# Kernel tuning notes

Measured on AMD Instinct MI355X. Metric: run time of the kernel, lower is better.

The kernel has to match this reference:

```python
import jax, jax.numpy as jnp
import numpy as np
import math

D = 2048
H = 16
DPH = 128          # d_pre_head (nope head dim, also dc_v)
DR = DPH // 2      # d_rope = 64
DC_V = DPH         # 128
DC_KV = DPH // 8   # 16
DC_Q = D // 4      # 512
QHD = DPH + DR     # 192
MEG = DPH + DC_V   # 256
B = 2
S = 2048
EPS = 1e-7


def setup_inputs() -> dict:
    key = jax.random.key(0)
    ks = jax.random.split(key, 8)
    sd = 0.02
    inputs = jax.random.normal(ks[0], (B, S, D), dtype=jnp.float32)
    pos_ids = jnp.tile(jnp.arange(S, dtype=jnp.int64 if jax.config.jax_enable_x64 else jnp.int32), (B, 1))
    mask = jnp.tril(jnp.ones((S, S), dtype=bool))  # causal: True = attend
    return {
        "inputs": inputs,
        "pos_ids": pos_ids,
        "mask": mask,
        "Wq_down": sd * jax.random.normal(ks[1], (D, DC_Q), jnp.float32),
        "q_norm_w": jnp.ones((DC_Q,), jnp.float32),
        "Wq_up": sd * jax.random.normal(ks[2], (DC_Q, H * QHD), jnp.float32),
        "Wkv_down": sd * jax.random.normal(ks[3], (D, DC_KV + DR), jnp.float32),
        "kv_norm_w": jnp.ones((DC_KV,), jnp.float32),
        "Wkv_up": sd * jax.random.normal(ks[4], (DC_KV, H * MEG), jnp.float32),
        "Wout": sd * jax.random.normal(ks[5], (H * DC_V, D), jnp.float32),
    }


def rms_norm(x, w):
    xf = x.astype(jnp.float32)
    var = jnp.mean(xf * xf, axis=-1, keepdims=True)
    return w * (xf * jax.lax.rsqrt(var + EPS)).astype(x.dtype)


def rope_reshape(x):
    # interleaved -> half-split layout: (..., d//2, 2) -> (..., 2, d//2) -> (..., d)
    *lead, d = x.shape
    return jnp.swapaxes(x.reshape(*lead, d // 2, 2), -1, -2).reshape(*lead, d)


def rope_rotate(x):
    h = x.shape[-1] // 2
    return jnp.concatenate([-x[..., h:], x[..., :h]], axis=-1)


def make_cos_sin(pos_ids):
    # pos_ids: [B, S] -> cos/sin: [B, 1, S, DR]
    inv_freq = 1.0 / (10000.0 ** (jnp.arange(0, DR, 2, dtype=jnp.float32) / DR))
    freqs = pos_ids[..., None].astype(jnp.float32) * inv_freq  # [B,S,DR/2]
    emb = jnp.concatenate([freqs, freqs], axis=-1)             # [B,S,DR]
    return jnp.cos(emb)[:, None], jnp.sin(emb)[:, None]


def reference(inputs, pos_ids, mask, Wq_down, q_norm_w, Wq_up, Wkv_down, kv_norm_w, Wkv_up, Wout):
    b, s, _ = inputs.shape
    # Q low-rank path
    q = rms_norm(inputs @ Wq_down, q_norm_w) @ Wq_up                 # [B,S,H*QHD]
    q = q.reshape(b, s, H, QHD).transpose(0, 2, 1, 3)                # [B,H,S,QHD]
    q_nope, q_rope = q[..., :DPH], q[..., DPH:]
    # KV low-rank path (shared latent + decoupled rope key)
    ckv = inputs @ Wkv_down                                          # [B,S,DC_KV+DR]
    c_kv, k_rope = ckv[..., :DC_KV], ckv[..., DC_KV:]
    c_kv = rms_norm(c_kv, kv_norm_w)
    kv = (c_kv @ Wkv_up).reshape(b, s, H, MEG).transpose(0, 2, 1, 3)  # [B,H,S,MEG]
    k_nope, value = kv[..., :DPH], kv[..., DPH:]
    k_rope = k_rope.reshape(b, s, 1, DR).transpose(0, 2, 1, 3)       # [B,1,S,DR]
    # RoPE on rope sub-dims only
    cos, sin = make_cos_sin(pos_ids)
    q_r = rope_reshape(q_rope)
    k_r = rope_reshape(k_rope)
    q_emb = q_r * cos + rope_rotate(q_r) * sin
    k_emb = k_r * cos + rope_rotate(k_r) * sin
    query = jnp.concatenate([q_nope, q_emb], axis=-1)                # [B,H,S,QHD]
    key = jnp.concatenate([k_nope, jnp.broadcast_to(k_emb, (b, H, s, DR))], axis=-1)
    # SDPA with default scale 1/sqrt(QHD), bool mask (True=keep)
    scores = jnp.einsum('bhqd,bhkd->bhqk', query, key) * (1.0 / math.sqrt(QHD))
    scores = jnp.where(mask, scores, -jnp.inf)
    attn = jax.nn.softmax(scores, axis=-1)
    out = jnp.einsum('bhqk,bhkv->bhqv', attn, value)                 # [B,H,S,DC_V]
    out = out.transpose(0, 2, 1, 3).reshape(b, s, H * DC_V)
    return out @ Wout                                                # [B,S,D]
```

## Files before the change

kernel.cpp:

```cpp
#include <hip/hip_runtime.h>

typedef __bf16 bf16;
typedef __bf16 bf16x8 __attribute__((ext_vector_type(8)));
typedef __bf16 bf16x4 __attribute__((ext_vector_type(4)));
typedef float f32x4 __attribute__((ext_vector_type(4)));

constexpr int D = 2048, H = 16, DPH = 128, DR = 64, DC_KV = 16, DC_Q = 512;
constexpr int QHD = 192, MEG = 256, B = 2, S = 2048;
constexpr int T = B * S;
constexpr int NDNP = 640;
constexpr int NQX = 1280;
constexpr float EPS = 1e-7f;
constexpr float KSC = 0.104124247f;

static __device__ __forceinline__ bf16x8 zero8() {
  bf16x8 v;
#pragma unroll
  for (int j = 0; j < 8; j++) v[j] = (bf16)0.f;
  return v;
}

static __device__ __forceinline__ void gload_lds16(const bf16* g, bf16* l) {
  __builtin_amdgcn_global_load_lds(
      (const __attribute__((address_space(1))) unsigned int*)g,
      (__attribute__((address_space(3))) unsigned int*)l, 16, 0, 0);
}

#define LGWAIT0 do { asm volatile("s_waitcnt lgkmcnt(0)" ::: "memory"); __builtin_amdgcn_sched_barrier(0); } while (0)
#define VMWAIT0 do { asm volatile("s_waitcnt vmcnt(0)" ::: "memory"); __builtin_amdgcn_sched_barrier(0); } while (0)

__global__ void rope_table_kernel(float* __restrict__ cos_t, float* __restrict__ sin_t) {
  int i = blockIdx.x * 64 + threadIdx.x;
  int pos = i >> 5, j = i & 31;
  double invf = pow(10000.0, -(double)(2 * j) / 64.0);
  double a = (double)pos * invf;
  cos_t[i] = (float)cos(a);
  sin_t[i] = (float)sin(a);
}

__global__ void zero_bf16_kernel(bf16* __restrict__ p, int n) {
  int i = (blockIdx.x * 256 + threadIdx.x) * 8;
  if (i < n) *reinterpret_cast<bf16x8*>(p + i) = zero8();
}

__global__ void cast_bf16_kernel(const float* __restrict__ in, bf16* __restrict__ out, int n) {
  int i = (blockIdx.x * blockDim.x + threadIdx.x) * 4;
  if (i < n) {
    float4 v = *reinterpret_cast<const float4*>(in + i);
    bf16x4 o;
    o[0] = (bf16)v.x; o[1] = (bf16)v.y; o[2] = (bf16)v.z; o[3] = (bf16)v.w;
    *reinterpret_cast<bf16x4*>(out + i) = o;
  }
}

__global__ __launch_bounds__(256) void transpose_cast_kernel(
    const float* __restrict__ in, bf16* __restrict__ out, int K, int N, int ldo) {
  __shared__ float tile[32][33];
  int k0 = blockIdx.y * 32, n0 = blockIdx.x * 32;
  int tid = threadIdx.x;
#pragma unroll
  for (int e = tid; e < 1024; e += 256) {
    int i = e >> 5, j = e & 31;
    int k = k0 + i, n = n0 + j;
    tile[i][j] = (k < K && n < N) ? in[(size_t)k * N + n] : 0.f;
  }
  __syncthreads();
#pragma unroll
  for (int e = tid; e < 1024; e += 256) {
    int jj = e >> 5, ii = e & 31;
    int n = n0 + jj, k = k0 + ii;
    if (k < K && n < N) out[(size_t)n * ldo + k] = (bf16)tile[ii][jj];
  }
}

__global__ __launch_bounds__(128) void prep_w2_kernel(
    const float* __restrict__ Wkv_up, const float* __restrict__ Wout,
    bf16* __restrict__ W2T) {
  __shared__ float wv[128][16];
  int h = blockIdx.y, d0 = blockIdx.x * 128;
  int tid = threadIdx.x;
#pragma unroll
  for (int e = tid; e < 2048; e += 128) {
    int v = e >> 4, c = e & 15;
    wv[v][c] = Wkv_up[(size_t)c * (H * MEG) + h * MEG + 128 + v];
  }
  __syncthreads();
  int d = d0 + tid;
  float acc[16] = {};
  for (int v = 0; v < 128; v++) {
    float wo = Wout[(size_t)(h * 128 + v) * D + d];
    float4 a0 = *reinterpret_cast<const float4*>(&wv[v][0]);
    float4 a1 = *reinterpret_cast<const float4*>(&wv[v][4]);
    float4 a2 = *reinterpret_cast<const float4*>(&wv[v][8]);
    float4 a3 = *reinterpret_cast<const float4*>(&wv[v][12]);
    acc[0] += a0.x * wo;  acc[1] += a0.y * wo;  acc[2] += a0.z * wo;  acc[3] += a0.w * wo;
    acc[4] += a1.x * wo;  acc[5] += a1.y * wo;  acc[6] += a1.z * wo;  acc[7] += a1.w * wo;
    acc[8] += a2.x * wo;  acc[9] += a2.y * wo;  acc[10] += a2.z * wo; acc[11] += a2.w * wo;
    acc[12] += a3.x * wo; acc[13] += a3.y * wo; acc[14] += a3.z * wo; acc[15] += a3.w * wo;
  }
  bf16x8 o0, o1;
#pragma unroll
  for (int c = 0; c < 8; c++) { o0[c] = (bf16)acc[c]; o1[c] = (bf16)acc[8 + c]; }
  *reinterpret_cast<bf16x8*>(&W2T[(size_t)d * 256 + h * 16]) = o0;
  *reinterpret_cast<bf16x8*>(&W2T[(size_t)d * 256 + h * 16 + 8]) = o1;
}

__global__ __launch_bounds__(128) void prep_w3_kernel(
    const float* __restrict__ Wq_up, const float* __restrict__ Wkv_up,
    bf16* __restrict__ WqxT) {
  __shared__ float wk[128][16];
  int h = blockIdx.y, k0 = blockIdx.x * 128;
  int tid = threadIdx.x;
#pragma unroll
  for (int e = tid; e < 2048; e += 128) {
    int v = e >> 4, c = e & 15;
    wk[v][c] = Wkv_up[(size_t)c * (H * MEG) + h * MEG + v];
  }
  __syncthreads();
  int k = k0 + tid;
  float acc[16] = {};
  for (int v = 0; v < 128; v++) {
    float wq = Wq_up[(size_t)k * (H * QHD) + h * QHD + v];
    float4 a0 = *reinterpret_cast<const float4*>(&wk[v][0]);
    float4 a1 = *reinterpret_cast<const float4*>(&wk[v][4]);
    float4 a2 = *reinterpret_cast<const float4*>(&wk[v][8]);
    float4 a3 = *reinterpret_cast<const float4*>(&wk[v][12]);
    acc[0] += a0.x * wq;  acc[1] += a0.y * wq;  acc[2] += a0.z * wq;  acc[3] += a0.w * wq;
    acc[4] += a1.x * wq;  acc[5] += a1.y * wq;  acc[6] += a1.z * wq;  acc[7] += a1.w * wq;
    acc[8] += a2.x * wq;  acc[9] += a2.y * wq;  acc[10] += a2.z * wq; acc[11] += a2.w * wq;
    acc[12] += a3.x * wq; acc[13] += a3.y * wq; acc[14] += a3.z * wq; acc[15] += a3.w * wq;
  }
#pragma unroll
  for (int c = 0; c < 16; c++)
    WqxT[(size_t)(h * 16 + c) * DC_Q + k] = (bf16)acc[c];
}

__global__ __launch_bounds__(256) void prep_wrope_kernel(
    const float* __restrict__ Wq_up, bf16* __restrict__ WqxT) {
  __shared__ float tile[64][65];
  int h = blockIdx.y, k0 = blockIdx.x * 64;
  int tid = threadIdx.x;
#pragma unroll
  for (int p = 0; p < 16; p++) {
    int kk = p * 4 + (tid >> 6), j = tid & 63;
    tile[kk][j] = Wq_up[(size_t)(k0 + kk) * (H * QHD) + h * QHD + 128 + j];
  }
  __syncthreads();
#pragma unroll
  for (int p = 0; p < 16; p++) {
    int n = p * 4 + (tid >> 6), k = tid & 63;
    WqxT[(size_t)(256 + h * 64 + n) * DC_Q + k0 + k] = (bf16)tile[k][n];
  }
}

__global__ __launch_bounds__(256) void rmsnorm_q_kernel(
    const float* __restrict__ cq, const float* __restrict__ w, bf16* __restrict__ outp, int ld) {
  int wid = threadIdx.x >> 6, lane = threadIdx.x & 63;
  int t = blockIdx.x * 4 + wid;
  const float* x = cq + (size_t)t * ld;
  float4 v0 = *reinterpret_cast<const float4*>(x + lane * 8);
  float4 v1 = *reinterpret_cast<const float4*>(x + lane * 8 + 4);
  float ss = v0.x * v0.x + v0.y * v0.y + v0.z * v0.z + v0.w * v0.w +
             v1.x * v1.x + v1.y * v1.y + v1.z * v1.z + v1.w * v1.w;
#pragma unroll
  for (int off = 32; off; off >>= 1) ss += __shfl_xor(ss, off);
  float r = rsqrtf(ss / (float)DC_Q + EPS);
  const float* wp = w + lane * 8;
  float vv[8] = {v0.x, v0.y, v0.z, v0.w, v1.x, v1.y, v1.z, v1.w};
  bf16x8 o;
#pragma unroll
  for (int j = 0; j < 8; j++) o[j] = (bf16)(vv[j] * r * wp[j]);
  *reinterpret_cast<bf16x8*>(outp + (size_t)t * DC_Q + lane * 8) = o;
}

__global__ __launch_bounds__(64) void kv_prep_kernel(
    const float* __restrict__ cqkv, const float* __restrict__ kvw,
    const int* __restrict__ pos_ids,
    const float* __restrict__ cos_t, const float* __restrict__ sin_t,
    bf16* __restrict__ KcG, bf16* __restrict__ cTG) {
  int t = blockIdx.x;
  int lane = threadIdx.x;
  int b = t >> 11, s = t & (S - 1);
  const float* x = cqkv + (size_t)t * NDNP + DC_Q;
  float v = (lane < 16) ? x[lane] : 0.f;
  float ss = v * v;
#pragma unroll
  for (int off = 1; off < 16; off <<= 1) ss += __shfl_xor(ss, off);
  float r = rsqrtf(ss / 16.f + EPS);
  bf16* krow = KcG + ((size_t)t << 7);
  if (lane < 16) {
    bf16 cn = (bf16)(v * r * kvw[lane]);
    krow[64 + lane] = cn;
    cTG[(size_t)(b * 16 + lane) * S + s] = cn;
  } else {
    krow[64 + lane] = (bf16)0.f;
  }
  if (lane < 32) {
    int j = lane;
    int pos = pos_ids[t];
    float cf = cos_t[pos * 32 + j], sf = sin_t[pos * 32 + j];
    float x0 = x[16 + 2 * j], x1 = x[16 + 2 * j + 1];
    krow[j]      = (bf16)(x0 * cf - x1 * sf);
    krow[32 + j] = (bf16)(x1 * cf + x0 * sf);
  }
}

__global__ __launch_bounds__(256) void build_q_kernel(
    const bf16* __restrict__ qx, const int* __restrict__ pos_ids,
    const float* __restrict__ cos_t, const float* __restrict__ sin_t,
    bf16* __restrict__ Qp) {
  int t = blockIdx.x;
  int b = t >> 11, s = t & (S - 1);
  int tid = threadIdx.x;
  int pos = pos_ids[t];
  const bf16* qr = qx + (size_t)t * NQX;
#pragma unroll
  for (int rep = 0; rep < 2; rep++) {
    int item = rep * 256 + tid;
    int h = item >> 5, j = item & 31;
    float cf = cos_t[pos * 32 + j], sf = sin_t[pos * 32 + j];
    float x0 = (float)qr[256 + h * 64 + 2 * j], x1 = (float)qr[256 + h * 64 + 2 * j + 1];
    bf16* qrow = Qp + (size_t)((b * 16 + h) * 2048 + s) * 96;
    qrow[j]      = (bf16)((x0 * cf - x1 * sf) * KSC);
    qrow[32 + j] = (bf16)((x1 * cf + x0 * sf) * KSC);
  }
  {
    int h = tid >> 4, c = tid & 15;
    bf16* qrow = Qp + (size_t)((b * 16 + h) * 2048 + s) * 96;
    qrow[64 + c] = (bf16)((float)qr[h * 16 + c] * KSC);
    qrow[80 + c] = (bf16)0.f;
  }
}

template <typename OutT>
__global__ __launch_bounds__(256) void gemm_bt_kernel(
    const bf16* __restrict__ A, const bf16* __restrict__ Bt,
    OutT* __restrict__ C, int M, int N, int K) {
  __shared__ bf16 As[2][64 * 64];
  __shared__ bf16 Bs[2][128 * 64];
  int tid = threadIdx.x;
  int wid = tid >> 6, lane = tid & 63;
  int g = lane >> 4, c = lane & 15;
  int nbx = gridDim.x;
  int lin = blockIdx.y * nbx + blockIdx.x;
  int cpx = (nbx * gridDim.y) >> 3;
  int swz = (lin & 7) * cpx + (lin >> 3);
  int m0 = (swz / nbx) * 64, n0 = (swz % nbx) * 128;
  int lrow8 = tid >> 3, lslot = tid & 7;

  auto stage = [&](int kt, int buf) {
    int k0 = kt << 6;
#pragma unroll
    for (int r = 0; r < 2; r++) {
      int row = r * 32 + lrow8;
      int sslot = lslot ^ (row & 7);
      gload_lds16(A + (size_t)(m0 + row) * K + k0 + sslot * 8, &As[buf][row * 64 + lslot * 8]);
    }
#pragma unroll
    for (int r = 0; r < 4; r++) {
      int row = r * 32 + lrow8;
      int sslot = lslot ^ (row & 7);
      gload_lds16(Bt + (size_t)(n0 + row) * K + k0 + sslot * 8, &Bs[buf][row * 64 + lslot * 8]);
    }
  };

  f32x4 acc[4][2] = {};
  int nk = K >> 6;
  stage(0, 0);
  __builtin_amdgcn_sched_barrier(0);
  for (int kt = 0; kt < nk; kt++) {
    int cur = kt & 1;
    __builtin_amdgcn_s_barrier();
    __builtin_amdgcn_sched_barrier(0);
    if (kt + 1 < nk) {
      stage(kt + 1, cur ^ 1);
      asm volatile("s_waitcnt vmcnt(6)" ::: "memory");
    } else {
      asm volatile("s_waitcnt vmcnt(0)" ::: "memory");
    }
    __builtin_amdgcn_sched_barrier(0);
    __builtin_amdgcn_s_barrier();
    __builtin_amdgcn_sched_barrier(0);
#pragma unroll
    for (int kk = 0; kk < 2; kk++) {
      bf16x8 af[4], bfr[2];
#pragma unroll
      for (int mi = 0; mi < 4; mi++) {
        int row = mi * 16 + c;
        int sl = (kk * 4 + g) ^ (row & 7);
        af[mi] = *reinterpret_cast<const bf16x8*>(&As[cur][row * 64 + sl * 8]);
      }
#pragma unroll
      for (int ni = 0; ni < 2; ni++) {
        int row = wid * 32 + ni * 16 + c;
        int sl = (kk * 4 + g) ^ (row & 7);
        bfr[ni] = *reinterpret_cast<const bf16x8*>(&Bs[cur][row * 64 + sl * 8]);
      }
#pragma unroll
      for (int mi = 0; mi < 4; mi++)
#pragma unroll
        for (int ni = 0; ni < 2; ni++)
          acc[mi][ni] = __builtin_amdgcn_mfma_f32_16x16x32_bf16(af[mi], bfr[ni], acc[mi][ni], 0, 0, 0);
    }
  }
#pragma unroll
  for (int mi = 0; mi < 4; mi++)
#pragma unroll
    for (int ni = 0; ni < 2; ni++)
#pragma unroll
      for (int r = 0; r < 4; r++) {
        int row = m0 + mi * 16 + g * 4 + r;
        int col = n0 + wid * 32 + ni * 16 + c;
        C[(size_t)row * N + col] = (OutT)acc[mi][ni][r];
      }
}

__global__ __launch_bounds__(512, 4) void attn_kernel(
    const bf16* __restrict__ Qp, const bf16* __restrict__ KcG,
    const bf16* __restrict__ cTG, bf16* __restrict__ OC) {
  __shared__ bf16 Kls[128 * 128];
  __shared__ bf16 Cls[2][16 * 128];
  __shared__ bf16 Pls[8][16 * 128];

  int lin = blockIdx.x;
  int v = lin >> 8, u = lin & 255;
  int qt = v ? (u >> 1) : (127 - (u >> 1));
  int hg = u & 1, b = v;
  int q0 = qt * 16;
  int nt = qt / 8 + 1;
  int tid = threadIdx.x;
  int w = tid >> 6, lane = tid & 63;
  int g = lane >> 4, cc = lane & 15;
  int h = hg * 8 + w;
  char* pbase = reinterpret_cast<char*>(&Pls[w][0]);

  bf16x8 kst[4];
  auto load_k = [&](int k0) {
#pragma unroll
    for (int i = 0; i < 4; i++) {
      int id = w * 4 + i;
      int key = id * 4 + (lane >> 4);
      int sg = (lane & 15) ^ ((id >> 1) & 15);
      kst[i] = *reinterpret_cast<const bf16x8*>(
          KcG + (((size_t)(b * S + k0 + key)) << 7) + sg * 8);
    }
  };
  auto write_k = [&]() {
#pragma unroll
    for (int i = 0; i < 4; i++) {
      int id = w * 4 + i;
      *reinterpret_cast<bf16x8*>(&Kls[(id * 64 + lane) * 8]) = kst[i];
    }
  };
  auto stage_c = [&](int k0, int buf) {
    if (w >= 4) {
      int c = (w - 4) * 4 + (lane >> 4);
      int sg = (lane & 15) ^ c;
      gload_lds16(cTG + (size_t)(b * 16 + c) * S + k0 + sg * 8,
                  &Cls[buf][(w - 4) * 512]);
    }
  };

  bf16x8 aq[3];
  const bf16* qp = Qp + (size_t)((b * 16 + h) * 2048 + q0 + cc) * 96;
#pragma unroll
  for (int kk = 0; kk < 3; kk++)
    aq[kk] = *reinterpret_cast<const bf16x8*>(qp + kk * 32 + g * 8);

  stage_c(0, 0);
  __builtin_amdgcn_sched_barrier(0);
  load_k(0);
  VMWAIT0;
  write_k();
  if (nt > 1) {
    stage_c(128, 1);
    __builtin_amdgcn_sched_barrier(0);
    load_k(128);
  }
  LGWAIT0;
  __builtin_amdgcn_s_barrier();
  __builtin_amdgcn_sched_barrier(0);

  bf16x8 ones;
#pragma unroll
  for (int j = 0; j < 8; j++) ones[j] = (bf16)1.f;

  f32x4 oc = {}, ls = {};

#pragma unroll 1
  for (int kt = 0; kt < nt; kt++) {
    int cur = kt & 1;
    int k0 = kt * 128;
    f32x4 sacc[8] = {};
    __builtin_amdgcn_s_setprio(1);
#pragma unroll
    for (int kk = 0; kk < 3; kk++)
#pragma unroll
      for (int ntb = 0; ntb < 8; ntb++) {
        int key = cc * 8 + ntb;
        bf16x8 bk = *reinterpret_cast<const bf16x8*>(
            &Kls[(key * 16 + ((kk * 4 + g) ^ cc)) * 8]);
        sacc[ntb] = __builtin_amdgcn_mfma_f32_16x16x32_bf16(aq[kk], bk, sacc[ntb], 0, 0, 0);
      }
    __builtin_amdgcn_s_setprio(0);

    bool diag = (kt == nt - 1);
#pragma unroll
    for (int r = 0; r < 4; r++) {
      bf16x8 pk;
#pragma unroll
      for (int ntb = 0; ntb < 8; ntb++) {
        float x = sacc[ntb][r];
        if (diag) {
          int qr = q0 + g * 4 + r, kc = k0 + cc * 8 + ntb;
          if (kc > qr) x = -1e30f;
        }
        pk[ntb] = (bf16)__builtin_amdgcn_exp2f(x);
      }
      int q = g * 4 + r;
      *reinterpret_cast<bf16x8*>(pbase + (q * 16 + (cc ^ (q & 7))) * 16) = pk;
    }
    LGWAIT0;
    __builtin_amdgcn_s_setprio(1);
#pragma unroll
    for (int kk2 = 0; kk2 < 4; kk2++) {
      bf16x8 pa = *reinterpret_cast<const bf16x8*>(
          pbase + (cc * 16 + ((kk2 * 4 + g) ^ (cc & 7))) * 16);
      bf16x8 bv = *reinterpret_cast<const bf16x8*>(
          &Cls[cur][(cc * 16 + ((kk2 * 4 + g) ^ cc)) * 8]);
      oc = __builtin_amdgcn_mfma_f32_16x16x32_bf16(pa, bv, oc, 0, 0, 0);
      ls = __builtin_amdgcn_mfma_f32_16x16x32_bf16(pa, ones, ls, 0, 0, 0);
    }
    __builtin_amdgcn_s_setprio(0);

    if (kt + 1 < nt) {
      __builtin_amdgcn_s_barrier();
      __builtin_amdgcn_sched_barrier(0);
      VMWAIT0;
      write_k();
      if (kt + 2 < nt) {
        stage_c((kt + 2) * 128, cur);
        __builtin_amdgcn_sched_barrier(0);
        load_k((kt + 2) * 128);
      }
      LGWAIT0;
      __builtin_amdgcn_s_barrier();
      __builtin_amdgcn_sched_barrier(0);
    }
  }

#pragma unroll
  for (int r = 0; r < 4; r++) {
    size_t t = (size_t)b * S + q0 + g * 4 + r;
    OC[t * 256 + h * 16 + cc] = (bf16)(oc[r] / ls[r]);
  }
}

extern "C" void kernel_launch(void* const* d_in, const int* in_sizes, int n_in,
                              void* d_out, int out_size, void* d_ws, size_t ws_size,
                              hipStream_t stream) {
  const float* inputs    = (const float*)d_in[0];
  const int*   pos_ids   = (const int*)d_in[1];
  const float* Wq_down   = (const float*)d_in[3];
  const float* q_norm_w  = (const float*)d_in[4];
  const float* Wq_up     = (const float*)d_in[5];
  const float* Wkv_down  = (const float*)d_in[6];
  const float* kv_norm_w = (const float*)d_in[7];
  const float* Wkv_up    = (const float*)d_in[8];
  const float* Wout      = (const float*)d_in[9];
  float* out = (float*)d_out;

  char* ws = (char*)d_ws;
  size_t off = 0;
  auto alloc = [&](size_t bytes) -> void* {
    void* p = ws + off;
    off += (bytes + 255) & ~(size_t)255;
    return p;
  };

  bf16*  in_bf = (bf16*)alloc((size_t)T * D * 2);
  bf16*  WdT   = (bf16*)alloc((size_t)NDNP * D * 2);
  bf16*  WqxT  = (bf16*)alloc((size_t)NQX * DC_Q * 2);
  bf16*  W2T   = (bf16*)alloc((size_t)D * 256 * 2);
  float* cqkv  = (float*)alloc((size_t)T * NDNP * 4);
  bf16*  cqn   = (bf16*)alloc((size_t)T * DC_Q * 2);
  bf16*  qx    = (bf16*)alloc((size_t)T * NQX * 2);
  bf16*  KcG   = (bf16*)alloc((size_t)T * 128 * 2);
  bf16*  cTG   = (bf16*)alloc((size_t)B * 16 * S * 2);
  bf16*  Qp    = (bf16*)alloc((size_t)B * H * S * 96 * 2);
  bf16*  OC    = (bf16*)alloc((size_t)T * H * 16 * 2);
  float* cos_t = (float*)alloc((size_t)S * 32 * 4);
  float* sin_t = (float*)alloc((size_t)S * 32 * 4);

  rope_table_kernel<<<S * 32 / 64, 64, 0, stream>>>(cos_t, sin_t);
  cast_bf16_kernel<<<(T * D / 4 + 255) / 256, 256, 0, stream>>>(inputs, in_bf, T * D);
  zero_bf16_kernel<<<(NDNP * D / 8 + 255) / 256, 256, 0, stream>>>(WdT, NDNP * D);
  transpose_cast_kernel<<<dim3((DC_Q + 31) / 32, (D + 31) / 32), 256, 0, stream>>>(Wq_down, WdT, D, DC_Q, D);
  transpose_cast_kernel<<<dim3((80 + 31) / 32, (D + 31) / 32), 256, 0, stream>>>(Wkv_down, WdT + (size_t)DC_Q * D, D, 80, D);
  prep_w3_kernel<<<dim3(4, 16), 128, 0, stream>>>(Wq_up, Wkv_up, WqxT);
  prep_wrope_kernel<<<dim3(8, 16), 256, 0, stream>>>(Wq_up, WqxT);
  prep_w2_kernel<<<dim3(16, 16), 128, 0, stream>>>(Wkv_up, Wout, W2T);

  gemm_bt_kernel<float><<<dim3(NDNP / 128, T / 64), 256, 0, stream>>>(in_bf, WdT, cqkv, T, NDNP, D);
  rmsnorm_q_kernel<<<T / 4, 256, 0, stream>>>(cqkv, q_norm_w, cqn, NDNP);
  kv_prep_kernel<<<T, 64, 0, stream>>>(cqkv, kv_norm_w, pos_ids, cos_t, sin_t, KcG, cTG);
  gemm_bt_kernel<bf16><<<dim3(NQX / 128, T / 64), 256, 0, stream>>>(cqn, WqxT, qx, T, NQX, DC_Q);
  build_q_kernel<<<T, 256, 0, stream>>>(qx, pos_ids, cos_t, sin_t, Qp);
  attn_kernel<<<512, 512, 0, stream>>>(Qp, KcG, cTG, OC);
  gemm_bt_kernel<float><<<dim3(D / 128, T / 64), 256, 0, stream>>>(OC, W2T, out, T, D, 256);
}
```

Measured before the change: 154.8 us.

## Merge prep kernels into one prologue and fuse RoPE Q-build into GEMM epilogue

Eight small weight-prep, cast and rope-table launches become a single prologue kernel that dispatches on block index. The Q rmsnorm and KV prep kernels are merged into one. The Q up-projection GEMM now applies RoPE and scaling in its epilogue and writes straight into the attention layout, so the qx intermediate and the build_q kernel go away. This cuts launch count and an HBM round trip, at the cost of scattered 2-byte epilogue stores and only partial zeroing of WdT.

```diff
diff --git a/kernel.cpp b/kernel.cpp
--- a/kernel.cpp
+++ b/kernel.cpp
@@ -29,135 +29,130 @@
 #define LGWAIT0 do { asm volatile("s_waitcnt lgkmcnt(0)" ::: "memory"); __builtin_amdgcn_sched_barrier(0); } while (0)
 #define VMWAIT0 do { asm volatile("s_waitcnt vmcnt(0)" ::: "memory"); __builtin_amdgcn_sched_barrier(0); } while (0)
 
-__global__ void rope_table_kernel(float* __restrict__ cos_t, float* __restrict__ sin_t) {
-  int i = blockIdx.x * 64 + threadIdx.x;
-  int pos = i >> 5, j = i & 31;
-  double invf = pow(10000.0, -(double)(2 * j) / 64.0);
-  double a = (double)pos * invf;
-  cos_t[i] = (float)cos(a);
-  sin_t[i] = (float)sin(a);
-}
-
-__global__ void zero_bf16_kernel(bf16* __restrict__ p, int n) {
-  int i = (blockIdx.x * 256 + threadIdx.x) * 8;
-  if (i < n) *reinterpret_cast<bf16x8*>(p + i) = zero8();
-}
-
-__global__ void cast_bf16_kernel(const float* __restrict__ in, bf16* __restrict__ out, int n) {
-  int i = (blockIdx.x * blockDim.x + threadIdx.x) * 4;
-  if (i < n) {
-    float4 v = *reinterpret_cast<const float4*>(in + i);
+__global__ __launch_bounds__(256) void prologue_kernel(
+    const float* __restrict__ inputs, const float* __restrict__ Wq_down,
+    const float* __restrict__ Wq_up, const float* __restrict__ Wkv_down,
+    const float* __restrict__ Wkv_up, const float* __restrict__ Wout,
+    bf16* __restrict__ in_bf, bf16* __restrict__ WdT, bf16* __restrict__ WqxT,
+    bf16* __restrict__ W2T, float* __restrict__ cos_t, float* __restrict__ sin_t) {
+  __shared__ float smem[64 * 65];
+  int bid = blockIdx.x;
+  int tid = threadIdx.x;
+
+  if (bid < 8192) {
+    int i = (bid * 256 + tid) * 4;
+    float4 v = *reinterpret_cast<const float4*>(inputs + i);
     bf16x4 o;
     o[0] = (bf16)v.x; o[1] = (bf16)v.y; o[2] = (bf16)v.z; o[3] = (bf16)v.w;
-    *reinterpret_cast<bf16x4*>(out + i) = o;
-  }
-}
-
-__global__ __launch_bounds__(256) void transpose_cast_kernel(
-    const float* __restrict__ in, bf16* __restrict__ out, int K, int N, int ldo) {
-  __shared__ float tile[32][33];
-  int k0 = blockIdx.y * 32, n0 = blockIdx.x * 32;
-  int tid = threadIdx.x;
-#pragma unroll
-  for (int e = tid; e < 1024; e += 256) {
-    int i = e >> 5, j = e & 31;
-    int k = k0 + i, n = n0 + j;
-    tile[i][j] = (k < K && n < N) ? in[(size_t)k * N + n] : 0.f;
-  }
-  __syncthreads();
-#pragma unroll
-  for (int e = tid; e < 1024; e += 256) {
-    int jj = e >> 5, ii = e & 31;
-    int n = n0 + jj, k = k0 + ii;
-    if (k < K && n < N) out[(size_t)n * ldo + k] = (bf16)tile[ii][jj];
-  }
-}
-
-__global__ __launch_bounds__(128) void prep_w2_kernel(
-    const float* __restrict__ Wkv_up, const float* __restrict__ Wout,
-    bf16* __restrict__ W2T) {
-  __shared__ float wv[128][16];
-  int h = blockIdx.y, d0 = blockIdx.x * 128;
-  int tid = threadIdx.x;
-#pragma unroll
-  for (int e = tid; e < 2048; e += 128) {
-    int v = e >> 4, c = e & 15;
-    wv[v][c] = Wkv_up[(size_t)c * (H * MEG) + h * MEG + 128 + v];
-  }
-  __syncthreads();
-  int d = d0 + tid;
-  float acc[16] = {};
-  for (int v = 0; v < 128; v++) {
-    float wo = Wout[(size_t)(h * 128 + v) * D + d];
-    float4 a0 = *reinterpret_cast<const float4*>(&wv[v][0]);
-    float4 a1 = *reinterpret_cast<const float4*>(&wv[v][4]);
-    float4 a2 = *reinterpret_cast<const float4*>(&wv[v][8]);
-    float4 a3 = *reinterpret_cast<const float4*>(&wv[v][12]);
-    acc[0] += a0.x * wo;  acc[1] += a0.y * wo;  acc[2] += a0.z * wo;  acc[3] += a0.w * wo;
-    acc[4] += a1.x * wo;  acc[5] += a1.y * wo;  acc[6] += a1.z * wo;  acc[7] += a1.w * wo;
-    acc[8] += a2.x * wo;  acc[9] += a2.y * wo;  acc[10] += a2.z * wo; acc[11] += a2.w * wo;
-    acc[12] += a3.x * wo; acc[13] += a3.y * wo; acc[14] += a3.z * wo; acc[15] += a3.w * wo;
-  }
-  bf16x8 o0, o1;
-#pragma unroll
-  for (int c = 0; c < 8; c++) { o0[c] = (bf16)acc[c]; o1[c] = (bf16)acc[8 + c]; }
-  *reinterpret_cast<bf16x8*>(&W2T[(size_t)d * 256 + h * 16]) = o0;
-  *reinterpret_cast<bf16x8*>(&W2T[(size_t)d * 256 + h * 16 + 8]) = o1;
-}
-
-__global__ __launch_bounds__(128) void prep_w3_kernel(
-    const float* __restrict__ Wq_up, const float* __restrict__ Wkv_up,
-    bf16* __restrict__ WqxT) {
-  __shared__ float wk[128][16];
-  int h = blockIdx.y, k0 = blockIdx.x * 128;
-  int tid = threadIdx.x;
-#pragma unroll
-  for (int e = tid; e < 2048; e += 128) {
-    int v = e >> 4, c = e & 15;
-    wk[v][c] = Wkv_up[(size_t)c * (H * MEG) + h * MEG + v];
-  }
-  __syncthreads();
-  int k = k0 + tid;
-  float acc[16] = {};
-  for (int v = 0; v < 128; v++) {
-    float wq = Wq_up[(size_t)k * (H * QHD) + h * QHD + v];
-    float4 a0 = *reinterpret_cast<const float4*>(&wk[v][0]);
-    float4 a1 = *reinterpret_cast<const float4*>(&wk[v][4]);
-    float4 a2 = *reinterpret_cast<const float4*>(&wk[v][8]);
-    float4 a3 = *reinterpret_cast<const float4*>(&wk[v][12]);
-    acc[0] += a0.x * wq;  acc[1] += a0.y * wq;  acc[2] += a0.z * wq;  acc[3] += a0.w * wq;
-    acc[4] += a1.x * wq;  acc[5] += a1.y * wq;  acc[6] += a1.z * wq;  acc[7] += a1.w * wq;
-    acc[8] += a2.x * wq;  acc[9] += a2.y * wq;  acc[10] += a2.z * wq; acc[11] += a2.w * wq;
-    acc[12] += a3.x * wq; acc[13] += a3.y * wq; acc[14] += a3.z * wq; acc[15] += a3.w * wq;
-  }
-#pragma unroll
-  for (int c = 0; c < 16; c++)
-    WqxT[(size_t)(h * 16 + c) * DC_Q + k] = (bf16)acc[c];
-}
-
-__global__ __launch_bounds__(256) void prep_wrope_kernel(
-    const float* __restrict__ Wq_up, bf16* __restrict__ WqxT) {
-  __shared__ float tile[64][65];
-  int h = blockIdx.y, k0 = blockIdx.x * 64;
-  int tid = threadIdx.x;
-#pragma unroll
-  for (int p = 0; p < 16; p++) {
-    int kk = p * 4 + (tid >> 6), j = tid & 63;
-    tile[kk][j] = Wq_up[(size_t)(k0 + kk) * (H * QHD) + h * QHD + 128 + j];
-  }
-  __syncthreads();
-#pragma unroll
-  for (int p = 0; p < 16; p++) {
-    int n = p * 4 + (tid >> 6), k = tid & 63;
-    WqxT[(size_t)(256 + h * 64 + n) * DC_Q + k0 + k] = (bf16)tile[k][n];
-  }
-}
-
-__global__ __launch_bounds__(256) void rmsnorm_q_kernel(
-    const float* __restrict__ cq, const float* __restrict__ w, bf16* __restrict__ outp, int ld) {
-  int wid = threadIdx.x >> 6, lane = threadIdx.x & 63;
-  int t = blockIdx.x * 4 + wid;
-  const float* x = cq + (size_t)t * ld;
+    *reinterpret_cast<bf16x4*>(in_bf + i) = o;
+  } else if (bid < 8240) {
+    size_t i = (size_t)592 * D + ((size_t)(bid - 8192) * 256 + tid) * 8;
+    *reinterpret_cast<bf16x8*>(WdT + i) = zero8();
+  } else if (bid < 9456) {
+    const float* src; bf16* dst; int K, N, k0, n0;
+    if (bid < 9264) {
+      int lb = bid - 8240;
+      src = Wq_down; dst = WdT; K = D; N = DC_Q;
+      k0 = (lb >> 4) * 32; n0 = (lb & 15) * 32;
+    } else {
+      int lb = bid - 9264;
+      src = Wkv_down; dst = WdT + (size_t)DC_Q * D; K = D; N = 80;
+      k0 = (lb / 3) * 32; n0 = (lb % 3) * 32;
+    }
+    float (*tile)[33] = (float(*)[33])smem;
+#pragma unroll
+    for (int e = tid; e < 1024; e += 256) {
+      int i = e >> 5, j = e & 31;
+      int k = k0 + i, n = n0 + j;
+      tile[i][j] = (k < K && n < N) ? src[(size_t)k * N + n] : 0.f;
+    }
+    __syncthreads();
+#pragma unroll
+    for (int e = tid; e < 1024; e += 256) {
+      int jj = e >> 5, ii = e & 31;
+      int n = n0 + jj, k = k0 + ii;
+      if (k < K && n < N) dst[(size_t)n * D + k] = (bf16)tile[ii][jj];
+    }
+  } else if (bid < 9520) {
+    int lb = bid - 9456;
+    int h = lb >> 2, k0 = (lb & 3) * 128;
+    float (*wk)[16] = (float(*)[16])smem;
+#pragma unroll
+    for (int e = tid; e < 2048; e += 256) {
+      int v = e >> 4, c = e & 15;
+      wk[v][c] = Wkv_up[(size_t)c * (H * MEG) + h * MEG + v];
+    }
+    __syncthreads();
+    if (tid < 128) {
+      int k = k0 + tid;
+      float acc[16] = {};
+      for (int v = 0; v < 128; v++) {
+        float wq = Wq_up[(size_t)k * (H * QHD) + h * QHD + v];
+#pragma unroll
+        for (int c = 0; c < 16; c++) acc[c] += wk[v][c] * wq;
+      }
+#pragma unroll
+      for (int c = 0; c < 16; c++)
+        WqxT[(size_t)(h * 16 + c) * DC_Q + k] = (bf16)acc[c];
+    }
+  } else if (bid < 9648) {
+    int lb = bid - 9520;
+    int h = lb >> 3, k0 = (lb & 7) * 64;
+    float (*tile)[65] = (float(*)[65])smem;
+#pragma unroll
+    for (int p = 0; p < 16; p++) {
+      int kk = p * 4 + (tid >> 6), j = tid & 63;
+      tile[kk][j] = Wq_up[(size_t)(k0 + kk) * (H * QHD) + h * QHD + 128 + j];
+    }
+    __syncthreads();
+#pragma unroll
+    for (int p = 0; p < 16; p++) {
+      int n = p * 4 + (tid >> 6), k = tid & 63;
+      WqxT[(size_t)(256 + h * 64 + n) * DC_Q + k0 + k] = (bf16)tile[k][n];
+    }
+  } else if (bid < 9904) {
+    int lb = bid - 9648;
+    int h = lb >> 4, d0 = (lb & 15) * 128;
+    float (*wv)[16] = (float(*)[16])smem;
+#pragma unroll
+    for (int e = tid; e < 2048; e += 256) {
+      int v = e >> 4, c = e & 15;
+      wv[v][c] = Wkv_up[(size_t)c * (H * MEG) + h * MEG + 128 + v];
+    }
+    __syncthreads();
+    if (tid < 128) {
+      int d = d0 + tid;
+      float acc[16] = {};
+      for (int v = 0; v < 128; v++) {
+        float wo = Wout[(size_t)(h * 128 + v) * D + d];
+#pragma unroll
+        for (int c = 0; c < 16; c++) acc[c] += wv[v][c] * wo;
+      }
+      bf16x8 o0, o1;
+#pragma unroll
+      for (int c = 0; c < 8; c++) { o0[c] = (bf16)acc[c]; o1[c] = (bf16)acc[8 + c]; }
+      *reinterpret_cast<bf16x8*>(&W2T[(size_t)d * 256 + h * 16]) = o0;
+      *reinterpret_cast<bf16x8*>(&W2T[(size_t)d * 256 + h * 16 + 8]) = o1;
+    }
+  } else {
+    int i = (bid - 9904) * 256 + tid;
+    int pos = i >> 5, j = i & 31;
+    double invf = pow(10000.0, -(double)(2 * j) / 64.0);
+    double a = (double)pos * invf;
+    cos_t[i] = (float)cos(a);
+    sin_t[i] = (float)sin(a);
+  }
+}
+
+__global__ __launch_bounds__(256) void norm_kv_kernel(
+    const float* __restrict__ cqkv, const float* __restrict__ qw,
+    const float* __restrict__ kvw, const int* __restrict__ pos_ids,
+    const float* __restrict__ cos_t, const float* __restrict__ sin_t,
+    bf16* __restrict__ cqn, bf16* __restrict__ KcG, bf16* __restrict__ cTG) {
+  int w = threadIdx.x >> 6, lane = threadIdx.x & 63;
+  int t = blockIdx.x * 4 + w;
+  int b = t >> 11, s = t & (S - 1);
+  const float* x = cqkv + (size_t)t * NDNP;
   float4 v0 = *reinterpret_cast<const float4*>(x + lane * 8);
   float4 v1 = *reinterpret_cast<const float4*>(x + lane * 8 + 4);
   float ss = v0.x * v0.x + v0.y * v0.y + v0.z * v0.z + v0.w * v0.w +
@@ -165,31 +160,21 @@
 #pragma unroll
   for (int off = 32; off; off >>= 1) ss += __shfl_xor(ss, off);
   float r = rsqrtf(ss / (float)DC_Q + EPS);
-  const float* wp = w + lane * 8;
+  const float* wp = qw + lane * 8;
   float vv[8] = {v0.x, v0.y, v0.z, v0.w, v1.x, v1.y, v1.z, v1.w};
   bf16x8 o;
 #pragma unroll
   for (int j = 0; j < 8; j++) o[j] = (bf16)(vv[j] * r * wp[j]);
-  *reinterpret_cast<bf16x8*>(outp + (size_t)t * DC_Q + lane * 8) = o;
-}
-
-__global__ __launch_bounds__(64) void kv_prep_kernel(
-    const float* __restrict__ cqkv, const float* __restrict__ kvw,
-    const int* __restrict__ pos_ids,
-    const float* __restrict__ cos_t, const float* __restrict__ sin_t,
-    bf16* __restrict__ KcG, bf16* __restrict__ cTG) {
-  int t = blockIdx.x;
-  int lane = threadIdx.x;
-  int b = t >> 11, s = t & (S - 1);
-  const float* x = cqkv + (size_t)t * NDNP + DC_Q;
-  float v = (lane < 16) ? x[lane] : 0.f;
-  float ss = v * v;
-#pragma unroll
-  for (int off = 1; off < 16; off <<= 1) ss += __shfl_xor(ss, off);
-  float r = rsqrtf(ss / 16.f + EPS);
+  *reinterpret_cast<bf16x8*>(cqn + (size_t)t * DC_Q + lane * 8) = o;
+  const float* xk = x + DC_Q;
+  float vk = (lane < 16) ? xk[lane] : 0.f;
+  float sk = vk * vk;
+#pragma unroll
+  for (int off = 1; off < 16; off <<= 1) sk += __shfl_xor(sk, off);
+  float rk = rsqrtf(sk / 16.f + EPS);
   bf16* krow = KcG + ((size_t)t << 7);
   if (lane < 16) {
-    bf16 cn = (bf16)(v * r * kvw[lane]);
+    bf16 cn = (bf16)(vk * rk * kvw[lane]);
     krow[64 + lane] = cn;
     cTG[(size_t)(b * 16 + lane) * S + s] = cn;
   } else {
@@ -199,43 +184,20 @@
     int j = lane;
     int pos = pos_ids[t];
     float cf = cos_t[pos * 32 + j], sf = sin_t[pos * 32 + j];
-    float x0 = x[16 + 2 * j], x1 = x[16 + 2 * j + 1];
+    float x0 = xk[16 + 2 * j], x1 = xk[16 + 2 * j + 1];
     krow[j]      = (bf16)(x0 * cf - x1 * sf);
     krow[32 + j] = (bf16)(x1 * cf + x0 * sf);
   }
 }
 
-__global__ __launch_bounds__(256) void build_q_kernel(
-    const bf16* __restrict__ qx, const int* __restrict__ pos_ids,
-    const float* __restrict__ cos_t, const float* __restrict__ sin_t,
-    bf16* __restrict__ Qp) {
-  int t = blockIdx.x;
-  int b = t >> 11, s = t & (S - 1);
-  int tid = threadIdx.x;
-  int pos = pos_ids[t];
-  const bf16* qr = qx + (size_t)t * NQX;
-#pragma unroll
-  for (int rep = 0; rep < 2; rep++) {
-    int item = rep * 256 + tid;
-    int h = item >> 5, j = item & 31;
-    float cf = cos_t[pos * 32 + j], sf = sin_t[pos * 32 + j];
-    float x0 = (float)qr[256 + h * 64 + 2 * j], x1 = (float)qr[256 + h * 64 + 2 * j + 1];
-    bf16* qrow = Qp + (size_t)((b * 16 + h) * 2048 + s) * 96;
-    qrow[j]      = (bf16)((x0 * cf - x1 * sf) * KSC);
-    qrow[32 + j] = (bf16)((x1 * cf + x0 * sf) * KSC);
-  }
-  {
-    int h = tid >> 4, c = tid & 15;
-    bf16* qrow = Qp + (size_t)((b * 16 + h) * 2048 + s) * 96;
-    qrow[64 + c] = (bf16)((float)qr[h * 16 + c] * KSC);
-    qrow[80 + c] = (bf16)0.f;
-  }
-}
-
-template <typename OutT>
+template <typename OutT, int EPI>
 __global__ __launch_bounds__(256) void gemm_bt_kernel(
     const bf16* __restrict__ A, const bf16* __restrict__ Bt,
-    OutT* __restrict__ C, int M, int N, int K) {
+    OutT* __restrict__ C, int M, int N, int K,
+    const int* __restrict__ pos_ids = nullptr,
+    const float* __restrict__ cos_t = nullptr,
+    const float* __restrict__ sin_t = nullptr,
+    bf16* __restrict__ Qp = nullptr) {
   __shared__ bf16 As[2][64 * 64];
   __shared__ bf16 Bs[2][128 * 64];
   int tid = threadIdx.x;
@@ -303,16 +265,51 @@
           acc[mi][ni] = __builtin_amdgcn_mfma_f32_16x16x32_bf16(af[mi], bfr[ni], acc[mi][ni], 0, 0, 0);
     }
   }
-#pragma unroll
-  for (int mi = 0; mi < 4; mi++)
-#pragma unroll
-    for (int ni = 0; ni < 2; ni++)
+
+  if constexpr (EPI == 0) {
+#pragma unroll
+    for (int mi = 0; mi < 4; mi++)
+#pragma unroll
+      for (int ni = 0; ni < 2; ni++)
+#pragma unroll
+        for (int r = 0; r < 4; r++) {
+          int row = m0 + mi * 16 + g * 4 + r;
+          int col = n0 + wid * 32 + ni * 16 + c;
+          C[(size_t)row * N + col] = (OutT)acc[mi][ni][r];
+        }
+  } else {
+    bool ropeTile = (n0 >= 256);
+#pragma unroll
+    for (int mi = 0; mi < 4; mi++)
 #pragma unroll
       for (int r = 0; r < 4; r++) {
         int row = m0 + mi * 16 + g * 4 + r;
-        int col = n0 + wid * 32 + ni * 16 + c;
-        C[(size_t)row * N + col] = (OutT)acc[mi][ni][r];
-      }
+        int b = row >> 11, s = row & (S - 1);
+#pragma unroll
+        for (int ni = 0; ni < 2; ni++) {
+          int col = n0 + wid * 32 + ni * 16 + c;
+          float val = acc[mi][ni][r];
+          if (!ropeTile) {
+            int h = col >> 4, cq = col & 15;
+            bf16* qrow = Qp + (size_t)((b * 16 + h) * 2048 + s) * 96;
+            qrow[64 + cq] = (bf16)(val * KSC);
+            qrow[80 + cq] = (bf16)0.f;
+          } else {
+            int colr = col - 256;
+            int h = colr >> 6, jj = colr & 63, j = jj >> 1;
+            int pos = pos_ids[row];
+            float cf = cos_t[pos * 32 + j], sf = sin_t[pos * 32 + j];
+            float other = __shfl_xor(val, 1);
+            bf16* qrow = Qp + (size_t)((b * 16 + h) * 2048 + s) * 96;
+            if ((c & 1) == 0) {
+              qrow[j] = (bf16)((val * cf - other * sf) * KSC);
+            } else {
+              qrow[32 + j] = (bf16)((val * cf + other * sf) * KSC);
+            }
+          }
+        }
+      }
+  }
 }
 
 __global__ __launch_bounds__(512, 4) void attn_kernel(
@@ -484,7 +481,6 @@
   bf16*  W2T   = (bf16*)alloc((size_t)D * 256 * 2);
   float* cqkv  = (float*)alloc((size_t)T * NDNP * 4);
   bf16*  cqn   = (bf16*)alloc((size_t)T * DC_Q * 2);
-  bf16*  qx    = (bf16*)alloc((size_t)T * NQX * 2);
   bf16*  KcG   = (bf16*)alloc((size_t)T * 128 * 2);
   bf16*  cTG   = (bf16*)alloc((size_t)B * 16 * S * 2);
   bf16*  Qp    = (bf16*)alloc((size_t)B * H * S * 96 * 2);
@@ -492,20 +488,17 @@
   float* cos_t = (float*)alloc((size_t)S * 32 * 4);
   float* sin_t = (float*)alloc((size_t)S * 32 * 4);
 
-  rope_table_kernel<<<S * 32 / 64, 64, 0, stream>>>(cos_t, sin_t);
-  cast_bf16_kernel<<<(T * D / 4 + 255) / 256, 256, 0, stream>>>(inputs, in_bf, T * D);
-  zero_bf16_kernel<<<(NDNP * D / 8 + 255) / 256, 256, 0, stream>>>(WdT, NDNP * D);
-  transpose_cast_kernel<<<dim3((DC_Q + 31) / 32, (D + 31) / 32), 256, 0, stream>>>(Wq_down, WdT, D, DC_Q, D);
-  transpose_cast_kernel<<<dim3((80 + 31) / 32, (D + 31) / 32), 256, 0, stream>>>(Wkv_down, WdT + (size_t)DC_Q * D, D, 80, D);
-  prep_w3_kernel<<<dim3(4, 16), 128, 0, stream>>>(Wq_up, Wkv_up, WqxT);
-  prep_wrope_kernel<<<dim3(8, 16), 256, 0, stream>>>(Wq_up, WqxT);
-  prep_w2_kernel<<<dim3(16, 16), 128, 0, stream>>>(Wkv_up, Wout, W2T);
-
-  gemm_bt_kernel<float><<<dim3(NDNP / 128, T / 64), 256, 0, stream>>>(in_bf, WdT, cqkv, T, NDNP, D);
-  rmsnorm_q_kernel<<<T / 4, 256, 0, stream>>>(cqkv, q_norm_w, cqn, NDNP);
-  kv_prep_kernel<<<T, 64, 0, stream>>>(cqkv, kv_norm_w, pos_ids, cos_t, sin_t, KcG, cTG);
-  gemm_bt_kernel<bf16><<<dim3(NQX / 128, T / 64), 256, 0, stream>>>(cqn, WqxT, qx, T, NQX, DC_Q);
-  build_q_kernel<<<T, 256, 0, stream>>>(qx, pos_ids, cos_t, sin_t, Qp);
+  prologue_kernel<<<10160, 256, 0, stream>>>(
+      inputs, Wq_down, Wq_up, Wkv_down, Wkv_up, Wout,
+      in_bf, WdT, WqxT, W2T, cos_t, sin_t);
+
+  gemm_bt_kernel<float, 0><<<dim3(NDNP / 128, T / 64), 256, 0, stream>>>(
+      in_bf, WdT, cqkv, T, NDNP, D);
+  norm_kv_kernel<<<T / 4, 256, 0, stream>>>(
+      cqkv, q_norm_w, kv_norm_w, pos_ids, cos_t, sin_t, cqn, KcG, cTG);
+  gemm_bt_kernel<bf16, 1><<<dim3(NQX / 128, T / 64), 256, 0, stream>>>(
+      cqn, WqxT, (bf16*)nullptr, T, NQX, DC_Q, pos_ids, cos_t, sin_t, Qp);
   attn_kernel<<<512, 512, 0, stream>>>(Qp, KcG, cTG, OC);
-  gemm_bt_kernel<float><<<dim3(D / 128, T / 64), 256, 0, stream>>>(OC, W2T, out, T, D, 256);
-}
+  gemm_bt_kernel<float, 0><<<dim3(D / 128, T / 64), 256, 0, stream>>>(
+      OC, W2T, out, T, D, 256);
+}
```

After: 136.5 us. -11.8%, faster.
